# Kernel optimization log

Hardware: AMD Instinct MI355X
Metric: run time of the kernel (lower is better)

The kernel has to match this reference:

```python
import jax, jax.numpy as jnp
import numpy as np
import math

B, C, TC, H, W = 8, 256, 512, 48, 48
EPS = 1e-6

def setup_inputs() -> dict:
    key = jax.random.key(0)
    kx, kt, kq, kk, kv = jax.random.split(key, 5)
    x = jax.random.normal(kx, (B, C, H, W), dtype=jnp.float32)
    token = jax.random.normal(kt, (B, TC, H, W), dtype=jnp.float32)
    # xavier_uniform for 1x1 conv weights [out, in]
    def xavier(k, fan_out, fan_in):
        a = math.sqrt(6.0 / (fan_in + fan_out))
        return jax.random.uniform(k, (fan_out, fan_in), dtype=jnp.float32, minval=-a, maxval=a)
    Wq = xavier(kq, C, C)
    Wk = xavier(kk, C, TC)
    Wv = xavier(kv, C, TC)
    alpha = jnp.float32(0.5)  # nonzero so the attention path affects the output
    return {"x": x, "token": token, "Wq": Wq, "Wk": Wk, "Wv": Wv, "alpha": alpha}

def reference(x, token, Wq, Wk, Wv, alpha):
    # 1x1 convs == per-pixel GEMMs over the channel dim
    q = jnp.einsum('oc,bchw->bohw', Wq, x)       # [B,C,H,W]
    k = jnp.einsum('oc,bchw->bohw', Wk, token)   # [B,C,H,W]
    v = jnp.einsum('oc,bchw->bohw', Wv, token)   # [B,C,H,W]
    b, c, h, w = q.shape
    n = h * w
    qf = q.reshape(b, c, n).transpose(0, 2, 1)   # [B,N,C]
    kf = k.reshape(b, c, n)                      # [B,C,N]
    vf = v.reshape(b, c, n).transpose(0, 2, 1)   # [B,N,C]
    # cosine normalization over the channel dim (F.normalize with eps clamp)
    qn = qf / jnp.maximum(jnp.linalg.norm(qf, axis=-1, keepdims=True), EPS)
    kn = kf / jnp.maximum(jnp.linalg.norm(kf, axis=1, keepdims=True), EPS)
    attn = jnp.einsum('bnc,bcm->bnm', qn, kn) / math.sqrt(c)  # [B,N,N]
    attn = jax.nn.softmax(attn, axis=-1)
    out = jnp.einsum('bnm,bmc->bnc', attn, vf)   # [B,N,C]
    out = out.transpose(0, 2, 1).reshape(b, c, h, w)
    return x + alpha * out
```

## Files before the change

### kernel.cpp

```cpp
#include <hip/hip_runtime.h>

#define B_   8
#define C_   256
#define TC_  512
#define HW_  2304
#define EPS_ 1e-6f

typedef __bf16 bf16_t;
typedef __bf16 bf16x8 __attribute__((ext_vector_type(8)));
typedef __bf16 bf16x4_t __attribute__((ext_vector_type(4)));
typedef float  f32x4 __attribute__((ext_vector_type(4)));
typedef unsigned int  u32;
typedef long long     i64;
typedef unsigned char u8;

__device__ __forceinline__ void g2l16(const void* g, void* l) {
    __builtin_amdgcn_global_load_lds(
        (const __attribute__((address_space(1))) unsigned int*)g,
        (__attribute__((address_space(3))) unsigned int*)l, 16, 0, 0);
}

__device__ __forceinline__ u8 to_fp8(float v) {
    return (u8)(__builtin_amdgcn_cvt_pk_fp8_f32(v, v, 0, false) & 0xff);
}

__global__ __launch_bounds__(256)
void wfrag_kernel(const float* __restrict__ wq, const float* __restrict__ wk,
                  const float* __restrict__ wv,
                  bf16_t* __restrict__ oq, bf16_t* __restrict__ ok,
                  bf16_t* __restrict__ ov)
{
    const int fid = blockIdx.x * 4 + (threadIdx.x >> 6);
    const int lane = threadIdx.x & 63;
    const int l16 = lane & 15, quad = lane >> 4;

    const float* src; bf16_t* dst; int cin, f;
    if (fid < 128)      { src = wq; dst = oq; cin = C_;  f = fid; }
    else if (fid < 384) { src = wk; dst = ok; cin = TC_; f = fid - 128; }
    else                { src = wv; dst = ov; cin = TC_; f = fid - 384; }
    const int nks = cin / 32;
    const int ot = f / nks, ks = f % nks;

    const float* s = src + (size_t)(ot * 16 + l16) * cin + ks * 32 + quad * 8;
    float4 a = *(const float4*)(s);
    float4 b = *(const float4*)(s + 4);
    bf16x8 o;
    o[0] = (__bf16)a.x; o[1] = (__bf16)a.y; o[2] = (__bf16)a.z; o[3] = (__bf16)a.w;
    o[4] = (__bf16)b.x; o[5] = (__bf16)b.y; o[6] = (__bf16)b.z; o[7] = (__bf16)b.w;
    *(bf16x8*)(dst + (size_t)f * 512 + lane * 8) = o;
}

template<int CIN, bool DO_V, bool KFMT>
__device__ __forceinline__ void conv_body(const float* __restrict__ X,
                                          const bf16_t* __restrict__ Wa,
                                          const bf16_t* __restrict__ Wvp,
                                          u8* __restrict__ outA, u8* __restrict__ outV,
                                          int bid, u8* smem)
{
    const int b  = bid & 7;
    const int n0 = (bid >> 3) * 16;
    const int tid = threadIdx.x;
    const int wv = tid >> 6;
    const int lane = tid & 63;
    const int quad = lane >> 4, l16 = lane & 15;
    const int NKS = CIN / 32;

    bf16_t (*T)[CIN + 8] = (bf16_t (*)[CIN + 8])smem;
    float (*ssp)[16] = (float (*)[16])(smem + (size_t)16 * (CIN + 8) * 2);

    {
        const float* Xb = X + (size_t)b * CIN * HW_ + n0;
        const int cl = tid >> 2;
        const int n4 = (tid & 3) * 4;
#pragma unroll
        for (int cp = 0; cp < CIN; cp += 64) {
            float4 v = *(const float4*)(Xb + (size_t)(cp + cl) * HW_ + n4);
            T[n4 + 0][cp + cl] = (__bf16)v.x;
            T[n4 + 1][cp + cl] = (__bf16)v.y;
            T[n4 + 2][cp + cl] = (__bf16)v.z;
            T[n4 + 3][cp + cl] = (__bf16)v.w;
        }
    }
    __syncthreads();

    bf16x8 af[CIN / 32];
#pragma unroll
    for (int ks = 0; ks < CIN / 32; ks++)
        af[ks] = *(const bf16x8*)(&T[l16][ks * 32 + quad * 8]);

    const int ot0 = wv * 4;

    f32x4 accK[4];
#pragma unroll
    for (int p = 0; p < 4; p++) accK[p] = (f32x4){0.f, 0.f, 0.f, 0.f};
    {
        const bf16_t* wbase = Wa + ((size_t)ot0 * NKS) * 512 + lane * 8;
#pragma unroll
        for (int ks = 0; ks < CIN / 32; ks++)
#pragma unroll
            for (int p = 0; p < 4; p++) {
                bf16x8 bw = *(const bf16x8*)(wbase + (size_t)(p * NKS + ks) * 512);
                accK[p] = __builtin_amdgcn_mfma_f32_16x16x32_bf16(af[ks], bw, accK[p], 0, 0, 0);
            }
    }

    {
        float ssr[4];
#pragma unroll
        for (int r = 0; r < 4; r++) {
            float ss = accK[0][r] * accK[0][r] + accK[1][r] * accK[1][r]
                     + accK[2][r] * accK[2][r] + accK[3][r] * accK[3][r];
            ss += __shfl_xor(ss, 1);
            ss += __shfl_xor(ss, 2);
            ss += __shfl_xor(ss, 4);
            ss += __shfl_xor(ss, 8);
            ssr[r] = ss;
        }
        if (l16 == 0) {
#pragma unroll
            for (int r = 0; r < 4; r++) ssp[wv][quad * 4 + r] = ssr[r];
        }
    }

    f32x4 accV[4];
    if (DO_V) {
#pragma unroll
        for (int p = 0; p < 4; p++) accV[p] = (f32x4){0.f, 0.f, 0.f, 0.f};
        const bf16_t* wbase = Wvp + ((size_t)ot0 * NKS) * 512 + lane * 8;
#pragma unroll
        for (int ks = 0; ks < CIN / 32; ks++)
#pragma unroll
            for (int p = 0; p < 4; p++) {
                bf16x8 aw = *(const bf16x8*)(wbase + (size_t)(p * NKS + ks) * 512);
                accV[p] = __builtin_amdgcn_mfma_f32_16x16x32_bf16(aw, af[ks], accV[p], 0, 0, 0);
            }
    }

    __syncthreads();

    float scale[4];
#pragma unroll
    for (int r = 0; r < 4; r++) {
        int px = quad * 4 + r;
        float s = ssp[0][px] + ssp[1][px] + ssp[2][px] + ssp[3][px];
        scale[r] = 1.0f / fmaxf(sqrtf(s), EPS_);
    }
    if (!KFMT) {
        u8* oa = outA + ((size_t)b * HW_ + n0 + quad * 4) * C_ + l16;
#pragma unroll
        for (int p = 0; p < 4; p++)
#pragma unroll
            for (int r = 0; r < 4; r++)
                oa[(size_t)r * C_ + (ot0 + p) * 16] = to_fp8(accK[p][r] * scale[r]);
    } else {
        u8* oa = outA + (size_t)b * 32 * HW_ * 8;
#pragma unroll
        for (int p = 0; p < 4; p++)
#pragma unroll
            for (int r = 0; r < 4; r++)
                oa[(((size_t)((ot0 + p) * 2 + (l16 >> 3))) * HW_
                    + n0 + quad * 4 + r) * 8 + (l16 & 7)]
                    = to_fp8(accK[p][r] * scale[r]);
    }

    if (DO_V) {
#pragma unroll
        for (int p = 0; p < 4; p++)
#pragma unroll
            for (int r = 0; r < 4; r++)
                outV[(((size_t)b * 288 + (n0 >> 3) + (l16 >> 3)) * 256
                      + (ot0 + p) * 16 + quad * 4 + r) * 8 + (l16 & 7)]
                    = to_fp8(accV[p][r]);
    }
}

__global__ __launch_bounds__(256, 4)
void convqkv_kernel(const float* __restrict__ x, const float* __restrict__ token,
                    const bf16_t* __restrict__ WqL, const bf16_t* __restrict__ WkL,
                    const bf16_t* __restrict__ WvL,
                    u8* __restrict__ q8, u8* __restrict__ k8, u8* __restrict__ v8)
{
    __shared__ __align__(16) u8 smem[16 * (TC_ + 8) * 2 + 256];
    const int NB1 = B_ * HW_ / 16;
    if ((int)blockIdx.x < NB1)
        conv_body<C_,  false, false>(x,     WqL, nullptr, q8, nullptr, blockIdx.x, smem);
    else
        conv_body<TC_, true,  true >(token, WkL, WvL,     k8, v8, blockIdx.x - NB1, smem);
}

__global__ __launch_bounds__(256, 3)
void attn_part_kernel(const u8* __restrict__ q8, const u8* __restrict__ k8,
                      const u8* __restrict__ v8,
                      bf16_t* __restrict__ Opart, float* __restrict__ lpart,
                      int tilesPerSplit, int JS)
{
    const int bid = blockIdx.x;
    const int b   = bid & 7;
    const int rr  = bid >> 3;
    const int js  = rr % JS;
    const int mt  = rr / JS;
    const int wv   = threadIdx.x >> 6;
    const int lane = threadIdx.x & 63;
    const int quad = lane >> 4;
    const int l16  = lane & 15;
    const int row0 = mt * 64 + wv * 16;
    const int jbase = js * tilesPerSplit * 32;

    const u8* qb = q8 + (size_t)b * HW_ * C_;
    const u8* kb = k8 + (size_t)b * 32 * HW_ * 8;
    const u8* vb = v8 + (size_t)b * 288 * 256 * 8;

    __shared__ u8 Kbuf[3][8192];
    __shared__ u8 Vbuf[3][8192];

    i64 aq[8];
    {
        const u8* r0 = qb + (size_t)(row0 + l16) * C_ + quad * 8;
#pragma unroll
        for (int t = 0; t < 8; t++) aq[t] = *(const i64*)(r0 + t * 32);
    }

    f32x4 O[16];
#pragma unroll
    for (int i = 0; i < 16; i++) O[i] = (f32x4){0.f, 0.f, 0.f, 0.f};
    float lsum = 0.f;

    const int sQuad = (lane >> 3) & 3;
    const int sRow2 = (lane & 7) * 2;
    const int sHi   = lane >> 5;

#define STAGE(bufi, j0g)                                                       \
    {                                                                          \
        _Pragma("unroll")                                                      \
        for (int p = 0; p < 2; p++) {                                          \
            int i = wv * 2 + p;                                                \
            g2l16(kb + ((size_t)(i * 4 + sQuad) * HW_                          \
                        + (j0g) + sRow2 + sHi * 16) * 8,                       \
                  &Kbuf[bufi][i * 1024]);                                      \
        }                                                                      \
        _Pragma("unroll")                                                      \
        for (int p = 0; p < 2; p++) {                                          \
            int i = wv * 2 + p;                                                \
            g2l16(vb + (((size_t)((j0g) >> 3) + sQuad) * 256                   \
                        + (2 * i + sHi) * 16 + sRow2) * 8,                     \
                  &Vbuf[bufi][i * 1024]);                                      \
        }                                                                      \
    }

    STAGE(0, jbase)
    STAGE(1, jbase + 32)

    const int roff = quad * 128 + l16 * 8;

    for (int tt = 0; tt < tilesPerSplit; tt++) {
        if (tt + 1 < tilesPerSplit) {
            asm volatile("s_waitcnt vmcnt(4)" ::: "memory");
        } else {
            asm volatile("s_waitcnt vmcnt(0)" ::: "memory");
        }
        __builtin_amdgcn_s_barrier();
        if (tt + 2 < tilesPerSplit)
            STAGE((tt + 2) % 3, jbase + (tt + 2) * 32)
        __builtin_amdgcn_sched_barrier(0);

        const u8* Kb = Kbuf[tt % 3];
        const u8* Vb = Vbuf[tt % 3];

        f32x4 s00 = (f32x4){0.f,0.f,0.f,0.f}, s01 = (f32x4){0.f,0.f,0.f,0.f};
        __builtin_amdgcn_s_setprio(1);
#pragma unroll
        for (int t = 0; t < 8; t++) {
            i64 bk0 = *(const i64*)(Kb + t * 1024 + roff);
            i64 bk1 = *(const i64*)(Kb + t * 1024 + roff + 512);
            s00 = __builtin_amdgcn_mfma_f32_16x16x32_fp8_fp8(bk0, aq[t], s00, 0, 0, 0);
            s01 = __builtin_amdgcn_mfma_f32_16x16x32_fp8_fp8(bk1, aq[t], s01, 0, 0, 0);
        }
        __builtin_amdgcn_s_setprio(0);

        float pA0 = __expf(s00[0] * 0.0625f), pA1 = __expf(s00[1] * 0.0625f);
        float pA2 = __expf(s00[2] * 0.0625f), pA3 = __expf(s00[3] * 0.0625f);
        float pB0 = __expf(s01[0] * 0.0625f), pB1 = __expf(s01[1] * 0.0625f);
        float pB2 = __expf(s01[2] * 0.0625f), pB3 = __expf(s01[3] * 0.0625f);
        lsum += (pA0 + pA1 + pA2 + pA3) + (pB0 + pB1 + pB2 + pB3);

        u32 A  = __builtin_amdgcn_cvt_pk_fp8_f32(pA0, pA1, 0, false);
        A      = __builtin_amdgcn_cvt_pk_fp8_f32(pA2, pA3, A, true);
        u32 Bw = __builtin_amdgcn_cvt_pk_fp8_f32(pB0, pB1, 0, false);
        Bw     = __builtin_amdgcn_cvt_pk_fp8_f32(pB2, pB3, Bw, true);

        asm volatile("v_permlane32_swap_b32 %0, %1" : "+v"(A), "+v"(Bw));
        asm volatile("v_permlane16_swap_b32 %0, %1" : "+v"(A), "+v"(Bw));
        i64 ap0 = ((i64)(u32)Bw << 32) | (i64)A;

        __builtin_amdgcn_s_setprio(1);
#pragma unroll
        for (int ct = 0; ct < 16; ct++) {
            i64 bv = *(const i64*)(Vb + ct * 512 + roff);
            O[ct] = __builtin_amdgcn_mfma_f32_16x16x32_fp8_fp8(ap0, bv, O[ct], 0, 0, 0);
        }
        __builtin_amdgcn_s_setprio(0);
    }

    lsum += __shfl_xor(lsum, 16);
    lsum += __shfl_xor(lsum, 32);
    float* lp = lpart + (size_t)(js * B_ + b) * HW_;
    if (quad == 0) lp[row0 + l16] = lsum;

    bf16_t* op = Opart + (size_t)(js * B_ + b) * C_ * HW_;
#pragma unroll
    for (int ct = 0; ct < 16; ct++) {
        int c = ct * 16 + l16;
        bf16x4_t v0;
        v0[0] = (__bf16)O[ct][0]; v0[1] = (__bf16)O[ct][1];
        v0[2] = (__bf16)O[ct][2]; v0[3] = (__bf16)O[ct][3];
        *(bf16x4_t*)(op + (size_t)c * HW_ + row0 + quad * 4) = v0;
    }
#undef STAGE
}

__global__ __launch_bounds__(256)
void epilogue_kernel(const float* __restrict__ x, const bf16_t* __restrict__ Opart,
                     const float* __restrict__ lpart, const float* __restrict__ alphaPtr,
                     float* __restrict__ out, int JS)
{
    const float a = *alphaPtr;
    const size_t S = (size_t)B_ * C_ * HW_;
    size_t flat = ((size_t)blockIdx.x * 256 + threadIdx.x) * 4;
    int bc = (int)(flat / HW_);
    int n  = (int)(flat % HW_);
    int b  = bc >> 8;
    float4 xv = *(const float4*)(x + flat);
    float s0 = 0.f, s1 = 0.f, s2 = 0.f, s3 = 0.f;
    float l0 = 0.f, l1 = 0.f, l2 = 0.f, l3 = 0.f;
    for (int js = 0; js < JS; js++) {
        bf16x4_t ov = *(const bf16x4_t*)(Opart + (size_t)js * S + flat);
        s0 += (float)ov[0]; s1 += (float)ov[1];
        s2 += (float)ov[2]; s3 += (float)ov[3];
        float4 lv = *(const float4*)(lpart + (size_t)(js * B_ + b) * HW_ + n);
        l0 += lv.x; l1 += lv.y; l2 += lv.z; l3 += lv.w;
    }
    float4 r;
    r.x = xv.x + a * s0 / l0;
    r.y = xv.y + a * s1 / l1;
    r.z = xv.z + a * s2 / l2;
    r.w = xv.w + a * s3 / l3;
    *(float4*)(out + flat) = r;
}

extern "C" void kernel_launch(void* const* d_in, const int* in_sizes, int n_in,
                              void* d_out, int out_size, void* d_ws, size_t ws_size,
                              hipStream_t stream)
{
    (void)in_sizes; (void)n_in; (void)out_size;
    const float* x     = (const float*)d_in[0];
    const float* token = (const float*)d_in[1];
    const float* Wq    = (const float*)d_in[2];
    const float* Wk    = (const float*)d_in[3];
    const float* Wv    = (const float*)d_in[4];
    const float* alpha = (const float*)d_in[5];
    float* out = (float*)d_out;

    const size_t S = (size_t)B_ * HW_ * C_;

    int JS = 4;
    for (;;) {
        size_t need = (12 + 2 * (size_t)JS) * S
                    + (size_t)JS * B_ * HW_ * 4 + (size_t)B_ * HW_ * 4;
        if (need <= ws_size || JS == 1) break;
        JS >>= 1;
    }
    const int tilesPerSplit = (HW_ / 32) / JS;

    char* ws = (char*)d_ws;
    bf16_t* WqL   = (bf16_t*)(ws + 6 * S);
    bf16_t* WkL   = WqL + (size_t)C_ * C_;
    bf16_t* WvL   = WkL + (size_t)C_ * TC_;
    u8*     q8    = (u8*)(ws + 7 * S);
    u8*     k8    = (u8*)(ws + 8 * S);
    u8*     v8    = (u8*)(ws + 9 * S);
    bf16_t* Opart = (bf16_t*)(ws + 12 * S);
    float*  lpart = (float*)(ws + (12 + 2 * (size_t)JS) * S);

    wfrag_kernel<<<dim3(160), dim3(256), 0, stream>>>(Wq, Wk, Wv, WqL, WkL, WvL);
    convqkv_kernel<<<dim3(2 * B_ * HW_ / 16), dim3(256), 0, stream>>>(x, token, WqL, WkL, WvL, q8, k8, v8);
    attn_part_kernel<<<dim3(JS * B_ * (HW_ / 64)), dim3(256), 0, stream>>>(q8, k8, v8, Opart, lpart, tilesPerSplit, JS);
    epilogue_kernel<<<dim3((int)(S / 1024)), dim3(256), 0, stream>>>(x, Opart, lpart, alpha, out, JS);
}
```

Baseline: 211.9 us.

## Fuse split-K epilogue into attention kernel via last-block atomic counter

Removes the separate epilogue kernel: each attention block bumps an atomic counter per (batch, row-tile), and the last split to finish reduces the partial outputs and row sums and writes x + alpha*out. The counters are zeroed in the weight-fragment kernel. This saves a kernel launch and lets the reduction overlap with attention blocks still running, at the cost of threadfences, an atomic per block, and a serialized tail in the last block of each tile.

```diff
diff --git a/kernel.cpp b/kernel.cpp
--- a/kernel.cpp
+++ b/kernel.cpp
@@ -28,8 +28,11 @@
 void wfrag_kernel(const float* __restrict__ wq, const float* __restrict__ wk,
                   const float* __restrict__ wv,
                   bf16_t* __restrict__ oq, bf16_t* __restrict__ ok,
-                  bf16_t* __restrict__ ov)
+                  bf16_t* __restrict__ ov, int* __restrict__ cnt)
 {
+    const int id = blockIdx.x * 256 + threadIdx.x;
+    if (id < 288) cnt[id] = 0;
+
     const int fid = blockIdx.x * 4 + (threadIdx.x >> 6);
     const int lane = threadIdx.x & 63;
     const int l16 = lane & 15, quad = lane >> 4;
@@ -192,6 +195,8 @@
 void attn_part_kernel(const u8* __restrict__ q8, const u8* __restrict__ k8,
                       const u8* __restrict__ v8,
                       bf16_t* __restrict__ Opart, float* __restrict__ lpart,
+                      const float* __restrict__ x, const float* __restrict__ alphaPtr,
+                      float* __restrict__ out, int* __restrict__ cnt,
                       int tilesPerSplit, int JS)
 {
     const int bid = blockIdx.x;
@@ -212,6 +217,7 @@
 
     __shared__ u8 Kbuf[3][8192];
     __shared__ u8 Vbuf[3][8192];
+    __shared__ int lastFlag;
 
     i64 aq[8];
     {
@@ -316,35 +322,47 @@
         *(bf16x4_t*)(op + (size_t)c * HW_ + row0 + quad * 4) = v0;
     }
 #undef STAGE
-}
-
-__global__ __launch_bounds__(256)
-void epilogue_kernel(const float* __restrict__ x, const bf16_t* __restrict__ Opart,
-                     const float* __restrict__ lpart, const float* __restrict__ alphaPtr,
-                     float* __restrict__ out, int JS)
-{
-    const float a = *alphaPtr;
-    const size_t S = (size_t)B_ * C_ * HW_;
-    size_t flat = ((size_t)blockIdx.x * 256 + threadIdx.x) * 4;
-    int bc = (int)(flat / HW_);
-    int n  = (int)(flat % HW_);
-    int b  = bc >> 8;
-    float4 xv = *(const float4*)(x + flat);
-    float s0 = 0.f, s1 = 0.f, s2 = 0.f, s3 = 0.f;
-    float l0 = 0.f, l1 = 0.f, l2 = 0.f, l3 = 0.f;
-    for (int js = 0; js < JS; js++) {
-        bf16x4_t ov = *(const bf16x4_t*)(Opart + (size_t)js * S + flat);
-        s0 += (float)ov[0]; s1 += (float)ov[1];
-        s2 += (float)ov[2]; s3 += (float)ov[3];
-        float4 lv = *(const float4*)(lpart + (size_t)(js * B_ + b) * HW_ + n);
-        l0 += lv.x; l1 += lv.y; l2 += lv.z; l3 += lv.w;
-    }
-    float4 r;
-    r.x = xv.x + a * s0 / l0;
-    r.y = xv.y + a * s1 / l1;
-    r.z = xv.z + a * s2 / l2;
-    r.w = xv.w + a * s3 / l3;
-    *(float4*)(out + flat) = r;
+
+    __syncthreads();
+    if (threadIdx.x == 0) {
+        __threadfence();
+        lastFlag = atomicAdd(&cnt[b * 36 + mt], 1);
+    }
+    __syncthreads();
+    if (lastFlag == JS - 1) {
+        __threadfence();
+        const int tid = threadIdx.x;
+        const int n4 = mt * 64 + (tid & 15) * 4;
+        float linv[4];
+        {
+            float l0 = 0.f, l1 = 0.f, l2 = 0.f, l3 = 0.f;
+            for (int j2 = 0; j2 < JS; j2++) {
+                float4 lv = *(const float4*)(lpart + (size_t)(j2 * B_ + b) * HW_ + n4);
+                l0 += lv.x; l1 += lv.y; l2 += lv.z; l3 += lv.w;
+            }
+            const float a = *alphaPtr;
+            linv[0] = a / l0; linv[1] = a / l1; linv[2] = a / l2; linv[3] = a / l3;
+        }
+        const int c0 = tid >> 4;
+        for (int cc = 0; cc < 16; cc++) {
+            int c = cc * 16 + c0;
+            size_t xo = ((size_t)b * C_ + c) * HW_ + n4;
+            float4 xv = *(const float4*)(x + xo);
+            float s0 = 0.f, s1 = 0.f, s2 = 0.f, s3 = 0.f;
+            for (int j2 = 0; j2 < JS; j2++) {
+                bf16x4_t ov = *(const bf16x4_t*)(Opart
+                    + ((size_t)(j2 * B_ + b) * C_ + c) * HW_ + n4);
+                s0 += (float)ov[0]; s1 += (float)ov[1];
+                s2 += (float)ov[2]; s3 += (float)ov[3];
+            }
+            float4 r;
+            r.x = xv.x + s0 * linv[0];
+            r.y = xv.y + s1 * linv[1];
+            r.z = xv.z + s2 * linv[2];
+            r.w = xv.w + s3 * linv[3];
+            *(float4*)(out + xo) = r;
+        }
+    }
 }
 
 extern "C" void kernel_launch(void* const* d_in, const int* in_sizes, int n_in,
@@ -378,11 +396,12 @@
     u8*     q8    = (u8*)(ws + 7 * S);
     u8*     k8    = (u8*)(ws + 8 * S);
     u8*     v8    = (u8*)(ws + 9 * S);
+    int*    cnt   = (int*)(ws + 10 * S);
     bf16_t* Opart = (bf16_t*)(ws + 12 * S);
     float*  lpart = (float*)(ws + (12 + 2 * (size_t)JS) * S);
 
-    wfrag_kernel<<<dim3(160), dim3(256), 0, stream>>>(Wq, Wk, Wv, WqL, WkL, WvL);
+    wfrag_kernel<<<dim3(160), dim3(256), 0, stream>>>(Wq, Wk, Wv, WqL, WkL, WvL, cnt);
     convqkv_kernel<<<dim3(2 * B_ * HW_ / 16), dim3(256), 0, stream>>>(x, token, WqL, WkL, WvL, q8, k8, v8);
-    attn_part_kernel<<<dim3(JS * B_ * (HW_ / 64)), dim3(256), 0, stream>>>(q8, k8, v8, Opart, lpart, tilesPerSplit, JS);
-    epilogue_kernel<<<dim3((int)(S / 1024)), dim3(256), 0, stream>>>(x, Opart, lpart, alpha, out, JS);
-}
+    attn_part_kernel<<<dim3(JS * B_ * (HW_ / 64)), dim3(256), 0, stream>>>(
+        q8, k8, v8, Opart, lpart, x, alpha, out, cnt, tilesPerSplit, JS);
+}
```

Measured after the change: 318.3 us. +50.2%, slower.
